# Kernel optimization log

Measured on AMD Instinct MI355X. Metric: run time of the kernel, lower is better.

## Reference

```python
import jax, jax.numpy as jnp
import numpy as np

B, T, C, H = 8, 2048, 1024, 64

def setup_inputs() -> dict:
    key = jax.random.key(0)
    k1, k2, k3, k4 = jax.random.split(key, 4)
    return {
        "inputs": jax.random.normal(k1, (B, T, C), dtype=jnp.float32),
        "Wq": jax.random.normal(k2, (C, H), dtype=jnp.float32) * (C ** -0.5),
        "Wk": jax.random.normal(k3, (C, H), dtype=jnp.float32) * (C ** -0.5),
        "Wv": jax.random.normal(k4, (C, H), dtype=jnp.float32) * (C ** -0.5),
    }

def reference(inputs, Wq, Wk, Wv):
    # q,k,v: [B,T,H]
    q = jnp.einsum('btc,ch->bth', inputs, Wq)
    k = jnp.einsum('btc,ch->bth', inputs, Wk)
    v = jnp.einsum('btc,ch->bth', inputs, Wv)
    c = inputs.shape[-1]
    # NOTE: original scales by C**-0.5 (embedding dim), not head_size**-0.5
    scale = jnp.asarray(c, inputs.dtype) ** -0.5
    wei = jnp.einsum('bqh,bkh->bqk', q, k) * scale  # [B,T,T]
    t = inputs.shape[1]
    causal = jnp.tril(jnp.ones((t, t), dtype=bool))
    wei = jnp.where(causal[None, :, :], wei, -jnp.inf)
    wei = jax.nn.softmax(wei, axis=-1)
    # dropout is identity in eval / DROP_RATE=0
    out = jnp.einsum('bqk,bkh->bqh', wei, v)  # [B,T,H]
    return out
```

## Files before the change

kernel.cpp:

```cpp
#include <hip/hip_runtime.h>
#include <stdint.h>

#define B_ 8
#define T_ 2048
#define C_ 1024
#define H_ 64
#define M_ (B_*T_)

typedef __bf16 bf16x8 __attribute__((ext_vector_type(8)));
typedef float  f32x4  __attribute__((ext_vector_type(4)));

union U4B { uint4 u; bf16x8 v; };

__device__ __forceinline__ unsigned short f32_to_bf16(float f) {
    union { float f; uint32_t u; } c; c.f = f;
    uint32_t u = c.u;
    u += 0x7fffu + ((u >> 16) & 1u);
    return (unsigned short)(u >> 16);
}
__device__ __forceinline__ uint32_t pack2_bf16(float a, float b) {
#if __has_builtin(__builtin_amdgcn_cvt_pk_bf16_f32)
    typedef __bf16 bf16x2 __attribute__((ext_vector_type(2)));
    union { bf16x2 v; uint32_t u; } c;
    c.v = __builtin_amdgcn_cvt_pk_bf16_f32(a, b);
    return c.u;
#else
    return (uint32_t)f32_to_bf16(a) | ((uint32_t)f32_to_bf16(b) << 16);
#endif
}

__global__ __launch_bounds__(256) void prepack_w(const float* __restrict__ Wq,
        const float* __restrict__ Wk, const float* __restrict__ Wv,
        unsigned short* __restrict__ wpk) {
    int o = blockIdx.x * 256 + threadIdx.x;
    if (o >= 24576) return;
    int lane = o & 63, nt = (o >> 6) % 12, kc = o / (64 * 12);
    int l15 = lane & 15, grp = lane >> 4;
    int n = nt * 16 + l15;
    int k = kc * 32 + grp * 8;
    const float* W = (n < 64) ? Wq : (n < 128) ? Wk : Wv;
    int col = n & 63;
    unsigned short tmp[8];
    #pragma unroll
    for (int j = 0; j < 8; j++) tmp[j] = f32_to_bf16(W[(size_t)(k + j) * 64 + col]);
    *(uint4*)(wpk + (size_t)o * 8) = *(uint4*)tmp;
}

__global__ __launch_bounds__(256) void qkv_kernel(const float* __restrict__ X,
        const unsigned short* __restrict__ wpk,
        unsigned short* __restrict__ qb, unsigned short* __restrict__ kb,
        unsigned short* __restrict__ vt) {
    __shared__ unsigned short Xl[32 * 1024];
    const int tid = threadIdx.x;
    const int wave = tid >> 6, lane = tid & 63;
    const int grp = lane >> 4, l15 = lane & 15;
    const int h = wave;
    const int t32 = blockIdx.x;

    const int rr = tid >> 4, ch = tid & 15;
    const int swzst = (rr & 7) << 4;

    #pragma unroll 2
    for (int s = 0; s < 2; s++) {
        const float* xrow = X + ((size_t)t32 * 32 + s * 16 + rr) * 1024 + ch * 8;
        float4 xa[8], xb[8];
        #pragma unroll
        for (int i = 0; i < 8; i++) {
            xa[i] = *(const float4*)(xrow + i * 128);
            xb[i] = *(const float4*)(xrow + i * 128 + 4);
        }
        char* xd = (char*)Xl + (s * 16 + rr) * 2048;
        #pragma unroll
        for (int i = 0; i < 8; i++) {
            uint4 pk = (uint4){ pack2_bf16(xa[i].x, xa[i].y), pack2_bf16(xa[i].z, xa[i].w),
                                pack2_bf16(xb[i].x, xb[i].y), pack2_bf16(xb[i].z, xb[i].w) };
            *(uint4*)(xd + ((ch * 16 + i * 256) ^ swzst)) = pk;
        }
    }

    const unsigned short* wp = wpk + ((size_t)(h * 3) * 64 + lane) * 8;
    uint4 w[4][3];
    #pragma unroll
    for (int d = 0; d < 4; d++)
        #pragma unroll
        for (int jj = 0; jj < 3; jj++)
            w[d][jj] = *(const uint4*)(wp + (size_t)(d * 768 + jj * 64) * 8);

    __syncthreads();

    f32x4 acc[2][3];
    #pragma unroll
    for (int m = 0; m < 2; m++)
        #pragma unroll
        for (int j = 0; j < 3; j++) acc[m][j] = (f32x4){0.f, 0.f, 0.f, 0.f};

    const char* xs0 = (const char*)Xl + l15 * 2048;
    const char* xs1 = (const char*)Xl + (16 + l15) * 2048;
    const int xswz = (l15 & 7) << 4;

    U4B ar[2][2];
    ar[0][0].u = *(const uint4*)(xs0 + ((grp * 16) ^ xswz));
    ar[0][1].u = *(const uint4*)(xs1 + ((grp * 16) ^ xswz));

    #pragma unroll
    for (int kc = 0; kc < 32; kc++) {
        const int cur = kc & 1, nxt = cur ^ 1;
        if (kc < 31) {
            ar[nxt][0].u = *(const uint4*)(xs0 + (((kc + 1) * 64 + grp * 16) ^ xswz));
            ar[nxt][1].u = *(const uint4*)(xs1 + (((kc + 1) * 64 + grp * 16) ^ xswz));
        }
        const int q = kc & 3;
        U4B b0, b1, b2;
        b0.u = w[q][0]; b1.u = w[q][1]; b2.u = w[q][2];
        acc[0][0] = __builtin_amdgcn_mfma_f32_16x16x32_bf16(ar[cur][0].v, b0.v, acc[0][0], 0, 0, 0);
        acc[0][1] = __builtin_amdgcn_mfma_f32_16x16x32_bf16(ar[cur][0].v, b1.v, acc[0][1], 0, 0, 0);
        acc[0][2] = __builtin_amdgcn_mfma_f32_16x16x32_bf16(ar[cur][0].v, b2.v, acc[0][2], 0, 0, 0);
        acc[1][0] = __builtin_amdgcn_mfma_f32_16x16x32_bf16(ar[cur][1].v, b0.v, acc[1][0], 0, 0, 0);
        acc[1][1] = __builtin_amdgcn_mfma_f32_16x16x32_bf16(ar[cur][1].v, b1.v, acc[1][1], 0, 0, 0);
        acc[1][2] = __builtin_amdgcn_mfma_f32_16x16x32_bf16(ar[cur][1].v, b2.v, acc[1][2], 0, 0, 0);
        if (kc + 4 < 32) {
            const unsigned short* wn = wp + (size_t)(kc + 4) * 768 * 8;
            #pragma unroll
            for (int jj = 0; jj < 3; jj++)
                w[q][jj] = *(const uint4*)(wn + jj * 64 * 8);
        }
    }

    #pragma unroll
    for (int m = 0; m < 2; m++) {
        const int r0 = t32 * 32 + m * 16 + grp * 4;
        const int bb = r0 >> 11;
        const int t0 = r0 & 2047;
        #pragma unroll
        for (int jj = 0; jj < 3; jj++) {
            int col = (h * 3 + jj) * 16 + l15;
            if (col < 64) {
                for (int r = 0; r < 4; r++)
                    qb[(size_t)(r0 + r) * 64 + col] = f32_to_bf16(acc[m][jj][r] * 0.03125f);
            } else if (col < 128) {
                for (int r = 0; r < 4; r++)
                    kb[(size_t)(r0 + r) * 64 + (col - 64)] = f32_to_bf16(acc[m][jj][r]);
            } else {
                int c = col - 128;
                ushort4 vv;
                vv.x = f32_to_bf16(acc[m][jj][0]); vv.y = f32_to_bf16(acc[m][jj][1]);
                vv.z = f32_to_bf16(acc[m][jj][2]); vv.w = f32_to_bf16(acc[m][jj][3]);
                *(ushort4*)(vt + ((size_t)bb * 64 + c) * 2048 + t0) = vv;
            }
        }
    }
}

__global__ __launch_bounds__(256) void attn1_kernel(const unsigned short* __restrict__ qb,
        const unsigned short* __restrict__ kb, const unsigned short* __restrict__ vt,
        float* __restrict__ pl, float* __restrict__ pacc) {
    __shared__ unsigned short Kl[64][72];
    __shared__ unsigned short Vl[64][72];
    const int tid = threadIdx.x;
    const int wave = tid >> 6, lane = tid & 63;
    const int grp = lane >> 4, l15 = lane & 15;
    const int b = blockIdx.x & 7;
    int f = blockIdx.x >> 3;
    int g = 0;
    for (; g < 32; g++) { int c = (39 - g) >> 3; if (f < c) break; f -= c; }
    const int j = 31 - g;
    const int s = f;
    const int ktend = min(8, (j + 1) - 8 * s);
    const int qbase = j * 64 + wave * 16;

    const unsigned short* qp = qb + ((size_t)b * 2048 + qbase + l15) * 64 + grp * 8;
    bf16x8 bq0 = *(const bf16x8*)qp;
    bf16x8 bq1 = *(const bf16x8*)(qp + 32);

    float lsum = 0.f;
    f32x4 acc[4];
    for (int d = 0; d < 4; d++) acc[d] = (f32x4){0.f, 0.f, 0.f, 0.f};

    const unsigned short* kB = kb + ((size_t)b * 2048 + s * 512) * 64;
    const unsigned short* vB = vt + (size_t)b * 64 * 2048 + s * 512;
    const int r1 = tid >> 3, c1 = (tid & 7) * 8;
    const int r2 = (tid + 256) >> 3, c2 = c1;

    uint4 kr0, kr1, vr0, vr1;
    kr0 = *(const uint4*)(kB + (size_t)r1 * 64 + c1);
    kr1 = *(const uint4*)(kB + (size_t)r2 * 64 + c2);
    vr0 = *(const uint4*)(vB + (size_t)r1 * 2048 + c1);
    vr1 = *(const uint4*)(vB + (size_t)r2 * 2048 + c2);

    for (int kt = 0; kt < ktend; kt++) {
        *(uint4*)&Kl[r1][c1] = kr0;  *(uint4*)&Kl[r2][c2] = kr1;
        *(uint4*)&Vl[r1][c1] = vr0;  *(uint4*)&Vl[r2][c2] = vr1;
        __syncthreads();
        if (kt + 1 < ktend) {
            const unsigned short* kN = kB + (size_t)(kt + 1) * 64 * 64;
            const unsigned short* vN = vB + (kt + 1) * 64;
            kr0 = *(const uint4*)(kN + (size_t)r1 * 64 + c1);
            kr1 = *(const uint4*)(kN + (size_t)r2 * 64 + c2);
            vr0 = *(const uint4*)(vN + (size_t)r1 * 2048 + c1);
            vr1 = *(const uint4*)(vN + (size_t)r2 * 2048 + c2);
        }
        const int keybase = s * 512 + kt * 64;
        f32x4 st[4];
        #pragma unroll
        for (int nt = 0; nt < 4; nt++) {
            bf16x8 a0 = *(const bf16x8*)&Kl[nt * 16 + l15][grp * 8];
            bf16x8 a1 = *(const bf16x8*)&Kl[nt * 16 + l15][32 + grp * 8];
            f32x4 t = (f32x4){0.f, 0.f, 0.f, 0.f};
            t = __builtin_amdgcn_mfma_f32_16x16x32_bf16(a0, bq0, t, 0, 0, 0);
            t = __builtin_amdgcn_mfma_f32_16x16x32_bf16(a1, bq1, t, 0, 0, 0);
            st[nt] = t;
        }
        if (keybase + 63 > qbase) {
            int q = qbase + l15;
            #pragma unroll
            for (int nt = 0; nt < 4; nt++)
                for (int r = 0; r < 4; r++)
                    if (keybase + nt * 16 + grp * 4 + r > q) st[nt][r] = -1e30f;
        }
        float p[4][4];
        #pragma unroll
        for (int nt = 0; nt < 4; nt++)
            for (int r = 0; r < 4; r++) { p[nt][r] = __expf(st[nt][r]); lsum += p[nt][r]; }
        uint32_t t0a = pack2_bf16(p[0][0], p[0][1]), t0b = pack2_bf16(p[0][2], p[0][3]);
        uint32_t t1a = pack2_bf16(p[1][0], p[1][1]), t1b = pack2_bf16(p[1][2], p[1][3]);
        uint32_t t2a = pack2_bf16(p[2][0], p[2][1]), t2b = pack2_bf16(p[2][2], p[2][3]);
        uint32_t t3a = pack2_bf16(p[3][0], p[3][1]), t3b = pack2_bf16(p[3][2], p[3][3]);
        const int s0l = ((grp & 1) << 5) + l15, s1l = s0l + 16;
        const bool hi = (grp >= 2);
        U4B bw0, bw1;
        {
            uint32_t e0a = (uint32_t)__shfl((int)t0a, s0l, 64);
            uint32_t e0b = (uint32_t)__shfl((int)t0b, s0l, 64);
            uint32_t e0c = (uint32_t)__shfl((int)t0a, s1l, 64);
            uint32_t e0d = (uint32_t)__shfl((int)t0b, s1l, 64);
            uint32_t e1a = (uint32_t)__shfl((int)t1a, s0l, 64);
            uint32_t e1b = (uint32_t)__shfl((int)t1b, s0l, 64);
            uint32_t e1c = (uint32_t)__shfl((int)t1a, s1l, 64);
            uint32_t e1d = (uint32_t)__shfl((int)t1b, s1l, 64);
            bw0.u = (uint4){ hi ? e1a : e0a, hi ? e1b : e0b, hi ? e1c : e0c, hi ? e1d : e0d };
        }
        {
            uint32_t e0a = (uint32_t)__shfl((int)t2a, s0l, 64);
            uint32_t e0b = (uint32_t)__shfl((int)t2b, s0l, 64);
            uint32_t e0c = (uint32_t)__shfl((int)t2a, s1l, 64);
            uint32_t e0d = (uint32_t)__shfl((int)t2b, s1l, 64);
            uint32_t e1a = (uint32_t)__shfl((int)t3a, s0l, 64);
            uint32_t e1b = (uint32_t)__shfl((int)t3b, s0l, 64);
            uint32_t e1c = (uint32_t)__shfl((int)t3a, s1l, 64);
            uint32_t e1d = (uint32_t)__shfl((int)t3b, s1l, 64);
            bw1.u = (uint4){ hi ? e1a : e0a, hi ? e1b : e0b, hi ? e1c : e0c, hi ? e1d : e0d };
        }
        #pragma unroll
        for (int dt = 0; dt < 4; dt++) {
            bf16x8 av0 = *(const bf16x8*)&Vl[dt * 16 + l15][grp * 8];
            bf16x8 av1 = *(const bf16x8*)&Vl[dt * 16 + l15][32 + grp * 8];
            acc[dt] = __builtin_amdgcn_mfma_f32_16x16x32_bf16(av0, bw0.v, acc[dt], 0, 0, 0);
            acc[dt] = __builtin_amdgcn_mfma_f32_16x16x32_bf16(av1, bw1.v, acc[dt], 0, 0, 0);
        }
        __syncthreads();
    }
    lsum += __shfl_xor(lsum, 16, 64);
    lsum += __shfl_xor(lsum, 32, 64);
    size_t rowq = (size_t)b * 2048 + qbase + l15;
    size_t p = rowq * 4 + s;
    if (grp == 0) pl[p] = lsum;
    #pragma unroll
    for (int dt = 0; dt < 4; dt++)
        *(f32x4*)&pacc[p * 64 + dt * 16 + grp * 4] = acc[dt];
}

__global__ __launch_bounds__(256) void attn2_kernel(const float* __restrict__ pl,
        const float* __restrict__ pacc, float* __restrict__ out) {
    int idx = blockIdx.x * 256 + threadIdx.x;
    int row = idx >> 4;
    int d0 = (idx & 15) * 4;
    int t = row & 2047;
    int ns = ((t >> 6) + 8) >> 3;
    float4 plv = *(const float4*)&pl[(size_t)row * 4];
    const float* pb = &pacc[(size_t)row * 4 * 64 + d0];
    f32x4 n0 = *(const f32x4*)(pb);
    f32x4 n1 = *(const f32x4*)(pb + 64);
    f32x4 n2 = *(const f32x4*)(pb + 128);
    f32x4 n3 = *(const f32x4*)(pb + 192);
    bool v1 = ns > 1, v2 = ns > 2, v3 = ns > 3;
    float den = plv.x + (v1 ? plv.y : 0.f) + (v2 ? plv.z : 0.f) + (v3 ? plv.w : 0.f);
    f32x4 num = n0;
    #pragma unroll
    for (int c = 0; c < 4; c++) {
        num[c] += v1 ? n1[c] : 0.f;
        num[c] += v2 ? n2[c] : 0.f;
        num[c] += v3 ? n3[c] : 0.f;
    }
    float inv = 1.f / den;
    *(f32x4*)&out[(size_t)row * 64 + d0] = num * inv;
}

extern "C" void kernel_launch(void* const* d_in, const int* in_sizes, int n_in,
                              void* d_out, int out_size, void* d_ws, size_t ws_size,
                              hipStream_t stream) {
    const float* X  = (const float*)d_in[0];
    const float* Wq = (const float*)d_in[1];
    const float* Wk = (const float*)d_in[2];
    const float* Wv = (const float*)d_in[3];
    float* out = (float*)d_out;

    unsigned short* qb  = (unsigned short*)d_ws;
    unsigned short* kb  = qb + (size_t)M_ * 64;
    unsigned short* wpk = kb + (size_t)M_ * 64;
    unsigned short* vt  = wpk + (size_t)24576 * 8;
    float* pl   = (float*)(vt + (size_t)B_ * 64 * 2048);
    float* pacc = pl + (size_t)M_ * 4;

    prepack_w<<<96, 256, 0, stream>>>(Wq, Wk, Wv, wpk);
    qkv_kernel<<<512, 256, 0, stream>>>(X, wpk, qb, kb, vt);
    attn1_kernel<<<640, 256, 0, stream>>>(qb, kb, vt, pl, pacc);
    attn2_kernel<<<1024, 256, 0, stream>>>(pl, pacc, out);
}
```

Baseline: 128.2 us.

## Fuse split-K attention reduction into attn1 via last-block atomic counter

Removes the separate attn2 combine kernel. Each attn1 block bumps a per-(batch, query-tile) counter after a threadfence, and the last split to finish sums the partial numerators and denominators and writes the output. The counters are zeroed inside prepack_w, so no extra launch is needed. This saves one kernel launch and lets the combine overlap with other attention blocks, at the cost of atomics, fences and a serialized tail in the last block of each tile.

Result: slower. 176.1 us (+37.4%).

```diff
diff --git a/kernel.cpp b/kernel.cpp
--- a/kernel.cpp
+++ b/kernel.cpp
@@ -31,8 +31,9 @@
 
 __global__ __launch_bounds__(256) void prepack_w(const float* __restrict__ Wq,
         const float* __restrict__ Wk, const float* __restrict__ Wv,
-        unsigned short* __restrict__ wpk) {
+        unsigned short* __restrict__ wpk, int* __restrict__ cnt) {
     int o = blockIdx.x * 256 + threadIdx.x;
+    if (o < 256) cnt[o] = 0;
     if (o >= 24576) return;
     int lane = o & 63, nt = (o >> 6) % 12, kc = o / (64 * 12);
     int l15 = lane & 15, grp = lane >> 4;
@@ -153,9 +154,11 @@
 
 __global__ __launch_bounds__(256) void attn1_kernel(const unsigned short* __restrict__ qb,
         const unsigned short* __restrict__ kb, const unsigned short* __restrict__ vt,
-        float* __restrict__ pl, float* __restrict__ pacc) {
+        float* __restrict__ pl, float* __restrict__ pacc,
+        float* __restrict__ out, int* __restrict__ cnt) {
     __shared__ unsigned short Kl[64][72];
     __shared__ unsigned short Vl[64][72];
+    __shared__ int lastflag;
     const int tid = threadIdx.x;
     const int wave = tid >> 6, lane = tid & 63;
     const int grp = lane >> 4, l15 = lane & 15;
@@ -267,32 +270,38 @@
     #pragma unroll
     for (int dt = 0; dt < 4; dt++)
         *(f32x4*)&pacc[p * 64 + dt * 16 + grp * 4] = acc[dt];
-}
-
-__global__ __launch_bounds__(256) void attn2_kernel(const float* __restrict__ pl,
-        const float* __restrict__ pacc, float* __restrict__ out) {
-    int idx = blockIdx.x * 256 + threadIdx.x;
-    int row = idx >> 4;
-    int d0 = (idx & 15) * 4;
-    int t = row & 2047;
-    int ns = ((t >> 6) + 8) >> 3;
-    float4 plv = *(const float4*)&pl[(size_t)row * 4];
-    const float* pb = &pacc[(size_t)row * 4 * 64 + d0];
-    f32x4 n0 = *(const f32x4*)(pb);
-    f32x4 n1 = *(const f32x4*)(pb + 64);
-    f32x4 n2 = *(const f32x4*)(pb + 128);
-    f32x4 n3 = *(const f32x4*)(pb + 192);
-    bool v1 = ns > 1, v2 = ns > 2, v3 = ns > 3;
-    float den = plv.x + (v1 ? plv.y : 0.f) + (v2 ? plv.z : 0.f) + (v3 ? plv.w : 0.f);
-    f32x4 num = n0;
-    #pragma unroll
-    for (int c = 0; c < 4; c++) {
-        num[c] += v1 ? n1[c] : 0.f;
-        num[c] += v2 ? n2[c] : 0.f;
-        num[c] += v3 ? n3[c] : 0.f;
-    }
-    float inv = 1.f / den;
-    *(f32x4*)&out[(size_t)row * 64 + d0] = num * inv;
+
+    __syncthreads();
+    if (tid == 0) {
+        __threadfence();
+        int old = atomicAdd(&cnt[b * 32 + j], 1);
+        lastflag = (old == ((j + 8) >> 3) - 1);
+    }
+    __syncthreads();
+    if (lastflag) {
+        __threadfence();
+        const int ns = (j + 8) >> 3;
+        const int r = tid >> 2, c0 = (tid & 3) * 16;
+        const size_t rq = (size_t)b * 2048 + j * 64 + r;
+        const float* pb = pacc + rq * 4 * 64;
+        float den = 0.f;
+        #pragma unroll
+        for (int s2 = 0; s2 < 4; s2++) {
+            float lv = pl[rq * 4 + s2];
+            den += (s2 < ns) ? lv : 0.f;
+        }
+        float inv = 1.f / den;
+        #pragma unroll
+        for (int cc = 0; cc < 4; cc++) {
+            f32x4 num = (f32x4){0.f, 0.f, 0.f, 0.f};
+            #pragma unroll
+            for (int s2 = 0; s2 < 4; s2++) {
+                f32x4 v = *(const f32x4*)(pb + s2 * 64 + c0 + cc * 4);
+                if (s2 < ns) num += v;
+            }
+            *(f32x4*)&out[rq * 64 + c0 + cc * 4] = num * inv;
+        }
+    }
 }
 
 extern "C" void kernel_launch(void* const* d_in, const int* in_sizes, int n_in,
@@ -310,9 +319,9 @@
     unsigned short* vt  = wpk + (size_t)24576 * 8;
     float* pl   = (float*)(vt + (size_t)B_ * 64 * 2048);
     float* pacc = pl + (size_t)M_ * 4;
-
-    prepack_w<<<96, 256, 0, stream>>>(Wq, Wk, Wv, wpk);
+    int*   cnt  = (int*)(pacc + (size_t)M_ * 4 * 64);
+
+    prepack_w<<<96, 256, 0, stream>>>(Wq, Wk, Wv, wpk, cnt);
     qkv_kernel<<<512, 256, 0, stream>>>(X, wpk, qb, kb, vt);
-    attn1_kernel<<<640, 256, 0, stream>>>(qb, kb, vt, pl, pacc);
-    attn2_kernel<<<1024, 256, 0, stream>>>(pl, pacc, out);
-}
+    attn1_kernel<<<640, 256, 0, stream>>>(qb, kb, vt, pl, pacc, out, cnt);
+}
```

## Load K and V fragments directly from global memory, dropping LDS staging

Applied to the files above, without the earlier changes.

The attention kernel no longer stages K and V tiles through shared memory with register prefetch and block barriers. Each wave now loads its MFMA operand fragments straight from global memory. This removes the LDS writes, LDS reads and both __syncthreads per tile. In exchange, each of the four waves fetches the same K/V data redundantly through the cache, and there is no longer explicit prefetch overlap of the next tile.

Result: slower. 156.4 us (+22.0%).

```diff
diff --git a/kernel.cpp b/kernel.cpp
--- a/kernel.cpp
+++ b/kernel.cpp
@@ -154,8 +154,6 @@
 __global__ __launch_bounds__(256) void attn1_kernel(const unsigned short* __restrict__ qb,
         const unsigned short* __restrict__ kb, const unsigned short* __restrict__ vt,
         float* __restrict__ pl, float* __restrict__ pacc) {
-    __shared__ unsigned short Kl[64][72];
-    __shared__ unsigned short Vl[64][72];
     const int tid = threadIdx.x;
     const int wave = tid >> 6, lane = tid & 63;
     const int grp = lane >> 4, l15 = lane & 15;
@@ -176,39 +174,32 @@
     f32x4 acc[4];
     for (int d = 0; d < 4; d++) acc[d] = (f32x4){0.f, 0.f, 0.f, 0.f};
 
-    const unsigned short* kB = kb + ((size_t)b * 2048 + s * 512) * 64;
-    const unsigned short* vB = vt + (size_t)b * 64 * 2048 + s * 512;
-    const int r1 = tid >> 3, c1 = (tid & 7) * 8;
-    const int r2 = (tid + 256) >> 3, c2 = c1;
-
-    uint4 kr0, kr1, vr0, vr1;
-    kr0 = *(const uint4*)(kB + (size_t)r1 * 64 + c1);
-    kr1 = *(const uint4*)(kB + (size_t)r2 * 64 + c2);
-    vr0 = *(const uint4*)(vB + (size_t)r1 * 2048 + c1);
-    vr1 = *(const uint4*)(vB + (size_t)r2 * 2048 + c2);
+    const unsigned short* kL = kb + ((size_t)b * 2048 + s * 512 + l15) * 64 + grp * 8;
+    const unsigned short* vL = vt + ((size_t)b * 64 + l15) * 2048 + s * 512 + grp * 8;
 
     for (int kt = 0; kt < ktend; kt++) {
-        *(uint4*)&Kl[r1][c1] = kr0;  *(uint4*)&Kl[r2][c2] = kr1;
-        *(uint4*)&Vl[r1][c1] = vr0;  *(uint4*)&Vl[r2][c2] = vr1;
-        __syncthreads();
-        if (kt + 1 < ktend) {
-            const unsigned short* kN = kB + (size_t)(kt + 1) * 64 * 64;
-            const unsigned short* vN = vB + (kt + 1) * 64;
-            kr0 = *(const uint4*)(kN + (size_t)r1 * 64 + c1);
-            kr1 = *(const uint4*)(kN + (size_t)r2 * 64 + c2);
-            vr0 = *(const uint4*)(vN + (size_t)r1 * 2048 + c1);
-            vr1 = *(const uint4*)(vN + (size_t)r2 * 2048 + c2);
-        }
         const int keybase = s * 512 + kt * 64;
+        U4B ka[4][2];
+        #pragma unroll
+        for (int nt = 0; nt < 4; nt++) {
+            const unsigned short* kr = kL + (size_t)(kt * 64 + nt * 16) * 64;
+            ka[nt][0].u = *(const uint4*)(kr);
+            ka[nt][1].u = *(const uint4*)(kr + 32);
+        }
         f32x4 st[4];
         #pragma unroll
         for (int nt = 0; nt < 4; nt++) {
-            bf16x8 a0 = *(const bf16x8*)&Kl[nt * 16 + l15][grp * 8];
-            bf16x8 a1 = *(const bf16x8*)&Kl[nt * 16 + l15][32 + grp * 8];
             f32x4 t = (f32x4){0.f, 0.f, 0.f, 0.f};
-            t = __builtin_amdgcn_mfma_f32_16x16x32_bf16(a0, bq0, t, 0, 0, 0);
-            t = __builtin_amdgcn_mfma_f32_16x16x32_bf16(a1, bq1, t, 0, 0, 0);
+            t = __builtin_amdgcn_mfma_f32_16x16x32_bf16(ka[nt][0].v, bq0, t, 0, 0, 0);
+            t = __builtin_amdgcn_mfma_f32_16x16x32_bf16(ka[nt][1].v, bq1, t, 0, 0, 0);
             st[nt] = t;
+        }
+        U4B va[4][2];
+        #pragma unroll
+        for (int dt = 0; dt < 4; dt++) {
+            const unsigned short* vr = vL + (size_t)(dt * 16) * 2048 + kt * 64;
+            va[dt][0].u = *(const uint4*)(vr);
+            va[dt][1].u = *(const uint4*)(vr + 32);
         }
         if (keybase + 63 > qbase) {
             int q = qbase + l15;
@@ -252,12 +243,9 @@
         }
         #pragma unroll
         for (int dt = 0; dt < 4; dt++) {
-            bf16x8 av0 = *(const bf16x8*)&Vl[dt * 16 + l15][grp * 8];
-            bf16x8 av1 = *(const bf16x8*)&Vl[dt * 16 + l15][32 + grp * 8];
-            acc[dt] = __builtin_amdgcn_mfma_f32_16x16x32_bf16(av0, bw0.v, acc[dt], 0, 0, 0);
-            acc[dt] = __builtin_amdgcn_mfma_f32_16x16x32_bf16(av1, bw1.v, acc[dt], 0, 0, 0);
-        }
-        __syncthreads();
+            acc[dt] = __builtin_amdgcn_mfma_f32_16x16x32_bf16(va[dt][0].v, bw0.v, acc[dt], 0, 0, 0);
+            acc[dt] = __builtin_amdgcn_mfma_f32_16x16x32_bf16(va[dt][1].v, bw1.v, acc[dt], 0, 0, 0);
+        }
     }
     lsum += __shfl_xor(lsum, 16, 64);
     lsum += __shfl_xor(lsum, 32, 64);
```
